# Kernel optimization log

Measured on AMD Instinct MI355X. Metric: run time of the kernel, lower is better.

## Reference

```python
import jax, jax.numpy as jnp
import numpy as np

T, N, E, F_IN, C = 8, 50000, 800000, 64, 64


def setup_inputs() -> dict:
    key = jax.random.key(0)
    ks = jax.random.split(key, 32)
    inp = {
        "x": jax.random.normal(ks[0], (T, N, F_IN), dtype=jnp.float32),
        "edge_index": jax.random.randint(ks[1], (2, E), 0, N, dtype=jnp.int32),
        "edge_weight": jax.random.uniform(ks[2], (E,), dtype=jnp.float32),
    }
    s = 0.05
    names = ["xz", "hz", "xr", "hr", "xh", "hh"]
    for i, nm in enumerate(names):
        cin = F_IN if nm[0] == "x" else C
        inp[f"W{nm}0"] = jax.random.normal(ks[3 + 3 * i], (cin, C), dtype=jnp.float32) * s
        inp[f"W{nm}1"] = jax.random.normal(ks[4 + 3 * i], (cin, C), dtype=jnp.float32) * s
        inp[f"b{nm}"] = jax.random.normal(ks[5 + 3 * i], (C,), dtype=jnp.float32) * s
    inp["W_lin"] = jax.random.normal(ks[30], (C, 1), dtype=jnp.float32) * s
    inp["b_lin"] = jax.random.normal(ks[31], (1,), dtype=jnp.float32) * s
    return inp


def reference(x, edge_index, edge_weight,
              Wxz0, Wxz1, bxz, Whz0, Whz1, bhz,
              Wxr0, Wxr1, bxr, Whr0, Whr1, bhr,
              Wxh0, Wxh1, bxh, Whh0, Whh1, bhh,
              W_lin, b_lin):
    src, dst = edge_index[0], edge_index[1]
    n = x.shape[1]
    # sym-normalized L_hat = -D^{-1/2} A D^{-1/2} (ChebConv, lambda_max=2)
    deg = jnp.zeros((n,), x.dtype).at[src].add(edge_weight)
    dinv = jnp.where(deg > 0, jax.lax.rsqrt(jnp.maximum(deg, 1e-12)), 0.0)
    nw = -edge_weight * dinv[src] * dinv[dst]  # (E,)

    def cheb(v, W0, W1, b):
        # K=2 Chebyshev: v @ W0 + (L_hat v) @ W1 + b ; v: (T, N, Cin)
        msgs = nw[None, :, None] * v[:, src, :]          # (T, E, Cin)
        tx1 = jnp.zeros_like(v).at[:, dst, :].add(msgs)  # scatter-add over nodes
        return v @ W0 + tx1 @ W1 + b

    H = jnp.zeros(x.shape[:2] + (Whz0.shape[0],), x.dtype)  # H=None -> zeros
    Z = jax.nn.sigmoid(cheb(x, Wxz0, Wxz1, bxz) + cheb(H, Whz0, Whz1, bhz))
    R = jax.nn.sigmoid(cheb(x, Wxr0, Wxr1, bxr) + cheb(H, Whr0, Whr1, bhr))
    Ht = jnp.tanh(cheb(x, Wxh0, Wxh1, bxh) + cheb(R * H, Whh0, Whh1, bhh))
    H = Z * H + (1.0 - Z) * Ht
    h = jax.nn.relu(H)
    return h @ W_lin + b_lin
```

## Files before the change

kernel.cpp:

```cpp
#include <hip/hip_runtime.h>

#define T_ 8
#define N_ 50000
#define E_ 800000
#define C_ 64
#define OVF_CAP 131072
#define NB 196
#define NBLK 256
#define EPB 3125
#define SCN (2 * NB * NBLK)
#define SCAN_TILES 49

typedef __attribute__((ext_vector_type(8))) short bf16x8;
typedef __attribute__((ext_vector_type(4))) float f32x4;

__device__ inline short f2bf(float f) {
    union { float f; unsigned int u; } v; v.f = f;
    unsigned int u = v.u + 0x7FFFu + ((v.u >> 16) & 1u);
    return (short)(u >> 16);
}
__device__ inline float bf2f_lo(unsigned int u) {
    union { unsigned int u; float f; } v; v.u = u << 16;
    return v.f;
}
__device__ inline float bf2f_hi(unsigned int u) {
    union { unsigned int u; float f; } v; v.u = u & 0xffff0000u;
    return v.f;
}

__device__ inline void xcvt_step(int id, const float* __restrict__ x,
                                 unsigned short* __restrict__ xb) {
    int c8 = id & 7;
    int t = (id >> 3) & 7;
    int n = id >> 6;
    const float* xr = x + ((long long)t * N_ + n) * C_ + c8 * 8;
    float4 a = *(const float4*)(xr);
    float4 b = *(const float4*)(xr + 4);
    bf16x8 o;
    o[0] = f2bf(a.x); o[1] = f2bf(a.y); o[2] = f2bf(a.z); o[3] = f2bf(a.w);
    o[4] = f2bf(b.x); o[5] = f2bf(b.y); o[6] = f2bf(b.z); o[7] = f2bf(b.w);
    *(bf16x8*)(xb + (long long)id * 8) = o;
}

__global__ __launch_bounds__(256) void prep_kernel(
        const int* __restrict__ src, const int* __restrict__ dst,
        int* __restrict__ counts,
        const float* __restrict__ x, unsigned short* __restrict__ xb,
        const float* __restrict__ Wz0, const float* __restrict__ Wz1,
        const float* __restrict__ Wh0, const float* __restrict__ Wh1,
        short* __restrict__ swz) {
    if (blockIdx.x < NBLK) {
        __shared__ int h[2 * NB];
        int t = threadIdx.x;
        for (int i = t; i < 2 * NB; i += 256) h[i] = 0;
        __syncthreads();
        int e0 = blockIdx.x * EPB;
        for (int j = t; j < EPB; j += 256) {
            int e = e0 + j;
            atomicAdd(&h[src[e] >> 8], 1);
            atomicAdd(&h[NB + (dst[e] >> 8)], 1);
        }
        __syncthreads();
        for (int i = t; i < 2 * NB; i += 256)
            counts[i * NBLK + blockIdx.x] = h[i];
    } else if (blockIdx.x < NBLK + 12500) {
        int id = (blockIdx.x - NBLK) * 256 + threadIdx.x;
        xcvt_step(id, x, xb);
    } else {
        int idx = (blockIdx.x - NBLK - 12500) * 256 + threadIdx.x;
        int j = idx & 7;
        int lane = (idx >> 3) & 63;
        int kb = (idx >> 9) & 1;
        int c = (idx >> 10) & 3;
        int mat = idx >> 12;
        const float* W = (mat == 0) ? Wz0 : (mat == 1) ? Wz1 : (mat == 2) ? Wh0 : Wh1;
        int k = kb * 32 + (lane >> 4) * 8 + j;
        int n = c * 16 + (lane & 15);
        swz[idx] = f2bf(W[k * 64 + n]);
    }
}

__global__ __launch_bounds__(1024) void scan_a_kernel(int* __restrict__ cnts,
                                                      int* __restrict__ tsum) {
    __shared__ int wsum[16];
    int tid = threadIdx.x, lane = tid & 63, wid = tid >> 6;
    int i0 = blockIdx.x * 2048 + tid * 2;
    int v0 = cnts[i0], v1 = cnts[i0 + 1];
    int orig = v0 + v1;
    int v = orig;
#pragma unroll
    for (int off = 1; off < 64; off <<= 1) {
        int u = __shfl_up(v, off);
        if (lane >= off) v += u;
    }
    if (lane == 63) wsum[wid] = v;
    __syncthreads();
    if (wid == 0) {
        int s = (lane < 16) ? wsum[lane] : 0;
#pragma unroll
        for (int off = 1; off < 16; off <<= 1) {
            int u = __shfl_up(s, off);
            if (lane >= off) s += u;
        }
        if (lane < 16) wsum[lane] = s;
    }
    __syncthreads();
    int wpre = wid ? wsum[wid - 1] : 0;
    int ex = wpre + v - orig;
    cnts[i0] = ex;
    cnts[i0 + 1] = ex + v0;
    if (tid == 0) tsum[blockIdx.x] = wsum[15];
}

__global__ __launch_bounds__(1024) void scan_b_kernel(const int* __restrict__ tsum,
                                                      int* __restrict__ cnts) {
    __shared__ int soff[SCAN_TILES];
    int tid = threadIdx.x, lane = tid & 63, wid = tid >> 6;
    if (wid == 0) {
        int own = (lane < SCAN_TILES) ? tsum[lane] : 0;
        int s = own;
#pragma unroll
        for (int off = 1; off < 64; off <<= 1) {
            int u = __shfl_up(s, off);
            if (lane >= off) s += u;
        }
        if (lane < SCAN_TILES) soff[lane] = s - own;
    }
    __syncthreads();
    int off = soff[blockIdx.x];
    int i0 = blockIdx.x * 2048 + tid;
    cnts[i0] += off;
    cnts[i0 + 1024] += off;
}

__global__ __launch_bounds__(256) void scatter_kernel(
        const int* __restrict__ src, const int* __restrict__ dst,
        const float* __restrict__ w, const int* __restrict__ scn,
        int2* __restrict__ rec) {
    __shared__ int offs[2 * NB];
    int t = threadIdx.x;
    for (int i = t; i < 2 * NB; i += 256)
        offs[i] = scn[i * NBLK + blockIdx.x];
    __syncthreads();
    int e0 = blockIdx.x * EPB;
    for (int j = t; j < EPB; j += 256) {
        int e = e0 + j;
        int s = src[e], d = dst[e];
        float wv = w[e];
        int r0 = atomicAdd(&offs[s >> 8], 1);
        rec[r0] = make_int2(s, __float_as_int(wv));
        int r1 = atomicAdd(&offs[NB + (d >> 8)], 1);
        rec[r1] = make_int2(s | ((d & 255) << 16), __float_as_int(wv));
    }
}

__global__ __launch_bounds__(256) void degw_kernel(
        const int2* __restrict__ rec, const int* __restrict__ scn,
        float* __restrict__ degw) {
    __shared__ float acc[256];
    int t = threadIdx.x, b = blockIdx.x;
    acc[t] = 0.f;
    __syncthreads();
    int s0 = scn[b * NBLK];
    int s1 = (b == NB - 1) ? E_ : scn[(b + 1) * NBLK];
    for (int j = s0 + t; j < s1; j += 256) {
        int2 r = rec[j];
        atomicAdd(&acc[r.x & 255], __int_as_float(r.y));
    }
    __syncthreads();
    int node = b * 256 + t;
    if (node < N_) degw[node] = acc[t];
}

__global__ __launch_bounds__(256) void esbuild_kernel(
        const int2* __restrict__ rec, const int* __restrict__ scn,
        const float* __restrict__ degw, int* __restrict__ cnt,
        int2* __restrict__ es, int cap,
        int* __restrict__ ovfcnt, int4* __restrict__ ovf) {
    __shared__ int cl[256];
    __shared__ float di[256];
    int t = threadIdx.x, b = blockIdx.x;
    cl[t] = 0;
    int node = b * 256 + t;
    float dd = (node < N_) ? degw[node] : 0.f;
    di[t] = dd > 0.f ? rsqrtf(fmaxf(dd, 1e-12f)) : 0.f;
    __syncthreads();
    int s0 = scn[(NB + b) * NBLK];
    int s1 = (b == NB - 1) ? 2 * E_ : scn[(NB + b + 1) * NBLK];
    for (int j = s0 + t; j < s1; j += 256) {
        int2 r = rec[j];
        int s = r.x & 0xffff;
        int dl = (r.x >> 16) & 255;
        float ds = degw[s];
        float is = ds > 0.f ? rsqrtf(fmaxf(ds, 1e-12f)) : 0.f;
        float nwv = -__int_as_float(r.y) * is * di[dl];
        int rank = atomicAdd(&cl[dl], 1);
        int d = b * 256 + dl;
        if (rank < cap) {
            es[d * cap + rank] = make_int2(s, __float_as_int(nwv));
        } else {
            int op = atomicAdd(ovfcnt, 1);
            if (op < OVF_CAP) ovf[op] = make_int4(d, s, __float_as_int(nwv), 0);
        }
    }
    __syncthreads();
    if (node < N_) cnt[node] = cl[t];
}

#define ACC8(W, V)                                                       \
    acc[0] += (W) * bf2f_lo((V).x); acc[1] += (W) * bf2f_hi((V).x);      \
    acc[2] += (W) * bf2f_lo((V).y); acc[3] += (W) * bf2f_hi((V).y);      \
    acc[4] += (W) * bf2f_lo((V).z); acc[5] += (W) * bf2f_hi((V).z);      \
    acc[6] += (W) * bf2f_lo((V).w); acc[7] += (W) * bf2f_hi((V).w);

__global__ __launch_bounds__(256) void gather_node_kernel(
        const int* __restrict__ cnt, const int2* __restrict__ es, int cap,
        const int* __restrict__ ovfcnt, const int4* __restrict__ ovf,
        const unsigned short* __restrict__ xb, const short* __restrict__ swz,
        const float* __restrict__ bxz, const float* __restrict__ bhz,
        const float* __restrict__ bxh, const float* __restrict__ bhh,
        const float* __restrict__ Wlin, const float* __restrict__ blin,
        float* __restrict__ out) {
    __shared__ unsigned short ltx[32 * 72];
    __shared__ float laz[2][16][65];

    int lane = threadIdx.x & 63;
    int wid = threadIdx.x >> 6;
    int base = blockIdx.x * 4;

    {
        int d = base + wid;
        int t = lane >> 3;
        int oct = lane & 7;
        int2 pk = (lane < cap) ? es[d * cap + lane] : make_int2(0, 0);
        int m = cnt[d];
        int mb = m < cap ? m : cap;

        float acc[8] = {0.f, 0.f, 0.f, 0.f, 0.f, 0.f, 0.f, 0.f};
        const unsigned short* xbase = xb + lane * 8;
        int k = 0;
        for (; k + 3 < mb; k += 4) {
            int s0 = __shfl(pk.x, k);
            int s1 = __shfl(pk.x, k + 1);
            int s2 = __shfl(pk.x, k + 2);
            int s3 = __shfl(pk.x, k + 3);
            uint4 v0 = *(const uint4*)(xbase + (long long)s0 * 512);
            uint4 v1 = *(const uint4*)(xbase + (long long)s1 * 512);
            uint4 v2 = *(const uint4*)(xbase + (long long)s2 * 512);
            uint4 v3 = *(const uint4*)(xbase + (long long)s3 * 512);
            float w0 = __int_as_float(__shfl(pk.y, k));
            float w1 = __int_as_float(__shfl(pk.y, k + 1));
            float w2 = __int_as_float(__shfl(pk.y, k + 2));
            float w3 = __int_as_float(__shfl(pk.y, k + 3));
            ACC8(w0, v0);
            ACC8(w1, v1);
            ACC8(w2, v2);
            ACC8(w3, v3);
        }
        for (; k < mb; ++k) {
            int s0 = __shfl(pk.x, k);
            float w0 = __int_as_float(__shfl(pk.y, k));
            uint4 v0 = *(const uint4*)(xbase + (long long)s0 * 512);
            ACC8(w0, v0);
        }
        if (m > cap) {
            int oc = *ovfcnt;
            if (oc > OVF_CAP) oc = OVF_CAP;
            for (int i = 0; i < oc; ++i) {
                int4 o = ovf[i];
                if (o.x == d) {
                    float w0 = __int_as_float(o.z);
                    uint4 v0 = *(const uint4*)(xbase + (long long)o.y * 512);
                    ACC8(w0, v0);
                }
            }
        }
        uint4 ob;
        ob.x = (unsigned int)(unsigned short)f2bf(acc[0]) |
               ((unsigned int)(unsigned short)f2bf(acc[1]) << 16);
        ob.y = (unsigned int)(unsigned short)f2bf(acc[2]) |
               ((unsigned int)(unsigned short)f2bf(acc[3]) << 16);
        ob.z = (unsigned int)(unsigned short)f2bf(acc[4]) |
               ((unsigned int)(unsigned short)f2bf(acc[5]) << 16);
        ob.w = (unsigned int)(unsigned short)f2bf(acc[6]) |
               ((unsigned int)(unsigned short)f2bf(acc[7]) << 16);
        int r = wid * 8 + t;
        *(uint4*)(ltx + r * 72 + oct * 8) = ob;
    }
    __syncthreads();

    int mt = wid >> 1;
    int g = wid & 1;
    int c16 = lane & 15;
    int kq = lane >> 4;
    int r_blk = mt * 16 + c16;
    const unsigned short* xr = xb + (long long)(base * 8 + r_blk) * C_ + kq * 8;
    bf16x8 ax0 = *(const bf16x8*)(xr);
    bf16x8 ax1 = *(const bf16x8*)(xr + 32);
    bf16x8 at0 = *(const bf16x8*)(ltx + r_blk * 72 + kq * 8);
    bf16x8 at1 = *(const bf16x8*)(ltx + r_blk * 72 + 32 + kq * 8);

    const float* bA = g ? bxh : bxz;
    const float* bB = g ? bhh : bhz;
    const short* wA = swz + (2 * g) * 4096 + lane * 8;
    const short* wB = swz + (2 * g + 1) * 4096 + lane * 8;

    f32x4 a4[4];
#pragma unroll
    for (int c = 0; c < 4; ++c) {
        int col = c * 16 + c16;
        float bv = bA[col] + bB[col];
        a4[c] = (f32x4){bv, bv, bv, bv};
    }
#pragma unroll
    for (int c = 0; c < 4; ++c) {
        bf16x8 bA0 = *(const bf16x8*)(wA + (c * 2 + 0) * 512);
        bf16x8 bA1 = *(const bf16x8*)(wA + (c * 2 + 1) * 512);
        bf16x8 bB0 = *(const bf16x8*)(wB + (c * 2 + 0) * 512);
        bf16x8 bB1 = *(const bf16x8*)(wB + (c * 2 + 1) * 512);
        a4[c] = __builtin_amdgcn_mfma_f32_16x16x32_bf16(ax0, bA0, a4[c], 0, 0, 0);
        a4[c] = __builtin_amdgcn_mfma_f32_16x16x32_bf16(ax1, bA1, a4[c], 0, 0, 0);
        a4[c] = __builtin_amdgcn_mfma_f32_16x16x32_bf16(at0, bB0, a4[c], 0, 0, 0);
        a4[c] = __builtin_amdgcn_mfma_f32_16x16x32_bf16(at1, bB1, a4[c], 0, 0, 0);
    }

    if (g == 0) {
#pragma unroll
        for (int c = 0; c < 4; ++c)
#pragma unroll
            for (int r = 0; r < 4; ++r)
                laz[mt][kq * 4 + r][c * 16 + c16] = a4[c][r];
    }
    __syncthreads();
    if (g == 1) {
        float part[4] = {0.f, 0.f, 0.f, 0.f};
#pragma unroll
        for (int c = 0; c < 4; ++c) {
            int col = c * 16 + c16;
            float wl = Wlin[col];
#pragma unroll
            for (int r = 0; r < 4; ++r) {
                float a = laz[mt][kq * 4 + r][col];
                float b = a4[c][r];
                float z = 1.f / (1.f + __expf(-a));
                float aa = fabsf(b);
                float e = __expf(-2.f * aa);
                float ht = copysignf((1.f - e) / (1.f + e), b);
                float h = fmaxf((1.f - z) * ht, 0.f);
                part[r] += h * wl;
            }
        }
#pragma unroll
        for (int m = 1; m <= 8; m <<= 1) {
#pragma unroll
            for (int r = 0; r < 4; ++r) part[r] += __shfl_xor(part[r], m);
        }
        if (c16 == 0) {
            float bl = blin[0];
#pragma unroll
            for (int r = 0; r < 4; ++r) {
                int rb = mt * 16 + kq * 4 + r;
                out[(long long)(rb & 7) * N_ + base + (rb >> 3)] = part[r] + bl;
            }
        }
    }
}

extern "C" void kernel_launch(void* const* d_in, const int* in_sizes, int n_in,
                              void* d_out, int out_size, void* d_ws, size_t ws_size,
                              hipStream_t stream) {
    const float* x    = (const float*)d_in[0];
    const int*   ei   = (const int*)d_in[1];
    const float* w    = (const float*)d_in[2];
    const float* Wxz0 = (const float*)d_in[3];
    const float* Wxz1 = (const float*)d_in[4];
    const float* bxz  = (const float*)d_in[5];
    const float* bhz  = (const float*)d_in[8];
    const float* Wxh0 = (const float*)d_in[15];
    const float* Wxh1 = (const float*)d_in[16];
    const float* bxh  = (const float*)d_in[17];
    const float* bhh  = (const float*)d_in[20];
    const float* Wlin = (const float*)d_in[21];
    const float* blin = (const float*)d_in[22];
    float* out = (float*)d_out;

    const int* src = ei;
    const int* dst = ei + E_;

    char* ws = (char*)d_ws;
    size_t off = 0;
    auto alloc = [&](size_t bytes) {
        char* p = ws + off;
        off = (off + bytes + 511) & ~(size_t)511;
        return p;
    };
    short* swz         = (short*)alloc(4 * 4096 * sizeof(short));
    float* degw        = (float*)alloc((size_t)N_ * 4);
    int*   cnt         = (int*)alloc((size_t)N_ * 4);
    int*   ovfcnt      = (int*)alloc(512);
    int4*  ovf         = (int4*)alloc((size_t)OVF_CAP * 16);
    int*   counts      = (int*)alloc((size_t)SCN * 4);
    int*   tsum        = (int*)alloc((size_t)SCAN_TILES * 4);
    int2*  rec         = (int2*)alloc((size_t)2 * E_ * 8);
    unsigned short* xb = (unsigned short*)alloc((size_t)T_ * N_ * C_ * 2);
    size_t fixed = off;

    int cap = 16;
    for (int c : {64, 48, 32, 24}) {
        if (fixed + (size_t)N_ * c * 8 + 512 <= ws_size) { cap = c; break; }
    }
    int2* es = (int2*)alloc((size_t)N_ * cap * 8);

    hipMemsetAsync(ovfcnt, 0, 4, stream);

    prep_kernel<<<NBLK + 12500 + 64, 256, 0, stream>>>(
        src, dst, counts, x, xb, Wxz0, Wxz1, Wxh0, Wxh1, swz);

    scan_a_kernel<<<SCAN_TILES, 1024, 0, stream>>>(counts, tsum);
    scan_b_kernel<<<SCAN_TILES, 1024, 0, stream>>>(tsum, counts);

    scatter_kernel<<<NBLK, 256, 0, stream>>>(src, dst, w, counts, rec);

    degw_kernel<<<NB, 256, 0, stream>>>(rec, counts, degw);

    esbuild_kernel<<<NB, 256, 0, stream>>>(rec, counts, degw, cnt,
                                           es, cap, ovfcnt, ovf);

    gather_node_kernel<<<N_ / 4, 256, 0, stream>>>(
        cnt, es, cap, ovfcnt, ovf, xb, swz,
        bxz, bhz, bxh, bhh, Wlin, blin, out);
}
```

Before: 368.1 us.

## Stage scatter records in LDS, widen preprocessing blocks, fold memset, split gather launch

The scatter kernel now builds a per-block local histogram and prefix sum, writes records into shared memory first, then copies them to global memory in bucket-contiguous runs. This turns random global writes into mostly coalesced ones. degw, esbuild and scatter move to 1024-thread blocks, the overflow counter reset is folded into scan_b in place of a separate memset, and the gather kernel is split into two half-size launches. The LDS staging buffer (about 50KB) limits occupancy, and the extra launch adds overhead.

```diff
diff --git a/kernel.cpp b/kernel.cpp
--- a/kernel.cpp
+++ b/kernel.cpp
@@ -113,9 +113,11 @@
 }
 
 __global__ __launch_bounds__(1024) void scan_b_kernel(const int* __restrict__ tsum,
-                                                      int* __restrict__ cnts) {
+                                                      int* __restrict__ cnts,
+                                                      int* __restrict__ ovfcnt) {
     __shared__ int soff[SCAN_TILES];
     int tid = threadIdx.x, lane = tid & 63, wid = tid >> 6;
+    if (blockIdx.x == 0 && tid == 0) *ovfcnt = 0;
     if (wid == 0) {
         int own = (lane < SCAN_TILES) ? tsum[lane] : 0;
         int s = own;
@@ -133,46 +135,83 @@
     cnts[i0 + 1024] += off;
 }
 
-__global__ __launch_bounds__(256) void scatter_kernel(
+__global__ __launch_bounds__(1024) void scatter_kernel(
         const int* __restrict__ src, const int* __restrict__ dst,
         const float* __restrict__ w, const int* __restrict__ scn,
         int2* __restrict__ rec) {
-    __shared__ int offs[2 * NB];
-    int t = threadIdx.x;
-    for (int i = t; i < 2 * NB; i += 256)
-        offs[i] = scn[i * NBLK + blockIdx.x];
-    __syncthreads();
-    int e0 = blockIdx.x * EPB;
-    for (int j = t; j < EPB; j += 256) {
+    __shared__ int h[512];
+    __shared__ int delta[512];
+    __shared__ int wsum[8];
+    __shared__ int2 lrec[2 * EPB];
+    int t = threadIdx.x, lane = t & 63, wid = t >> 6;
+    int c = blockIdx.x;
+    if (t < 512) h[t] = 0;
+    __syncthreads();
+    int e0 = c * EPB;
+    for (int j = t; j < EPB; j += 1024) {
+        int e = e0 + j;
+        atomicAdd(&h[src[e] >> 8], 1);
+        atomicAdd(&h[NB + (dst[e] >> 8)], 1);
+    }
+    __syncthreads();
+    int v = (t < 512) ? h[t] : 0;
+    int s2 = v;
+#pragma unroll
+    for (int off = 1; off < 64; off <<= 1) {
+        int u = __shfl_up(s2, off);
+        if (lane >= off) s2 += u;
+    }
+    if (lane == 63 && wid < 8) wsum[wid] = s2;
+    __syncthreads();
+    if (t == 0) {
+        int r = 0;
+#pragma unroll
+        for (int i = 0; i < 8; ++i) { int x2 = wsum[i]; wsum[i] = r; r += x2; }
+    }
+    __syncthreads();
+    int ex = (t < 512) ? (wsum[wid] + s2 - v) : 0;
+    int gb = (t < 2 * NB) ? scn[t * NBLK + c] : 0;
+    __syncthreads();
+    if (t < 512) { delta[t] = gb - ex; h[t] = ex; }
+    __syncthreads();
+    int lb196 = h[NB];
+    __syncthreads();
+    for (int j = t; j < EPB; j += 1024) {
         int e = e0 + j;
         int s = src[e], d = dst[e];
-        float wv = w[e];
-        int r0 = atomicAdd(&offs[s >> 8], 1);
-        rec[r0] = make_int2(s, __float_as_int(wv));
-        int r1 = atomicAdd(&offs[NB + (d >> 8)], 1);
-        rec[r1] = make_int2(s | ((d & 255) << 16), __float_as_int(wv));
-    }
-}
-
-__global__ __launch_bounds__(256) void degw_kernel(
+        int wv = __float_as_int(w[e]);
+        int p0 = atomicAdd(&h[s >> 8], 1);
+        lrec[p0] = make_int2(s, wv);
+        int p1 = atomicAdd(&h[NB + (d >> 8)], 1);
+        lrec[p1] = make_int2(s | ((d & 255) << 16) | ((d >> 8) << 24), wv);
+    }
+    __syncthreads();
+    for (int j = t; j < 2 * EPB; j += 1024) {
+        int2 r = lrec[j];
+        int i = (j >= lb196) ? (NB + ((unsigned)r.x >> 24)) : ((r.x & 0xffff) >> 8);
+        rec[delta[i] + j] = r;
+    }
+}
+
+__global__ __launch_bounds__(1024) void degw_kernel(
         const int2* __restrict__ rec, const int* __restrict__ scn,
         float* __restrict__ degw) {
     __shared__ float acc[256];
     int t = threadIdx.x, b = blockIdx.x;
-    acc[t] = 0.f;
+    if (t < 256) acc[t] = 0.f;
     __syncthreads();
     int s0 = scn[b * NBLK];
-    int s1 = (b == NB - 1) ? E_ : scn[(b + 1) * NBLK];
-    for (int j = s0 + t; j < s1; j += 256) {
+    int s1 = scn[(b + 1) * NBLK];
+    for (int j = s0 + t; j < s1; j += 1024) {
         int2 r = rec[j];
         atomicAdd(&acc[r.x & 255], __int_as_float(r.y));
     }
     __syncthreads();
     int node = b * 256 + t;
-    if (node < N_) degw[node] = acc[t];
-}
-
-__global__ __launch_bounds__(256) void esbuild_kernel(
+    if (t < 256 && node < N_) degw[node] = acc[t];
+}
+
+__global__ __launch_bounds__(1024) void esbuild_kernel(
         const int2* __restrict__ rec, const int* __restrict__ scn,
         const float* __restrict__ degw, int* __restrict__ cnt,
         int2* __restrict__ es, int cap,
@@ -180,14 +219,16 @@
     __shared__ int cl[256];
     __shared__ float di[256];
     int t = threadIdx.x, b = blockIdx.x;
-    cl[t] = 0;
     int node = b * 256 + t;
-    float dd = (node < N_) ? degw[node] : 0.f;
-    di[t] = dd > 0.f ? rsqrtf(fmaxf(dd, 1e-12f)) : 0.f;
+    if (t < 256) {
+        cl[t] = 0;
+        float dd = (node < N_) ? degw[node] : 0.f;
+        di[t] = dd > 0.f ? rsqrtf(fmaxf(dd, 1e-12f)) : 0.f;
+    }
     __syncthreads();
     int s0 = scn[(NB + b) * NBLK];
     int s1 = (b == NB - 1) ? 2 * E_ : scn[(NB + b + 1) * NBLK];
-    for (int j = s0 + t; j < s1; j += 256) {
+    for (int j = s0 + t; j < s1; j += 1024) {
         int2 r = rec[j];
         int s = r.x & 0xffff;
         int dl = (r.x >> 16) & 255;
@@ -204,7 +245,7 @@
         }
     }
     __syncthreads();
-    if (node < N_) cnt[node] = cl[t];
+    if (t < 256 && node < N_) cnt[node] = cl[t];
 }
 
 #define ACC8(W, V)                                                       \
@@ -220,13 +261,13 @@
         const float* __restrict__ bxz, const float* __restrict__ bhz,
         const float* __restrict__ bxh, const float* __restrict__ bhh,
         const float* __restrict__ Wlin, const float* __restrict__ blin,
-        float* __restrict__ out) {
+        float* __restrict__ out, int boff) {
     __shared__ unsigned short ltx[32 * 72];
     __shared__ float laz[2][16][65];
 
     int lane = threadIdx.x & 63;
     int wid = threadIdx.x >> 6;
-    int base = blockIdx.x * 4;
+    int base = (blockIdx.x + boff) * 4;
 
     {
         int d = base + wid;
@@ -411,22 +452,23 @@
     }
     int2* es = (int2*)alloc((size_t)N_ * cap * 8);
 
-    hipMemsetAsync(ovfcnt, 0, 4, stream);
-
     prep_kernel<<<NBLK + 12500 + 64, 256, 0, stream>>>(
         src, dst, counts, x, xb, Wxz0, Wxz1, Wxh0, Wxh1, swz);
 
     scan_a_kernel<<<SCAN_TILES, 1024, 0, stream>>>(counts, tsum);
-    scan_b_kernel<<<SCAN_TILES, 1024, 0, stream>>>(tsum, counts);
-
-    scatter_kernel<<<NBLK, 256, 0, stream>>>(src, dst, w, counts, rec);
-
-    degw_kernel<<<NB, 256, 0, stream>>>(rec, counts, degw);
-
-    esbuild_kernel<<<NB, 256, 0, stream>>>(rec, counts, degw, cnt,
-                                           es, cap, ovfcnt, ovf);
-
-    gather_node_kernel<<<N_ / 4, 256, 0, stream>>>(
+    scan_b_kernel<<<SCAN_TILES, 1024, 0, stream>>>(tsum, counts, ovfcnt);
+
+    scatter_kernel<<<NBLK, 1024, 0, stream>>>(src, dst, w, counts, rec);
+
+    degw_kernel<<<NB, 1024, 0, stream>>>(rec, counts, degw);
+
+    esbuild_kernel<<<NB, 1024, 0, stream>>>(rec, counts, degw, cnt,
+                                            es, cap, ovfcnt, ovf);
+
+    gather_node_kernel<<<6250, 256, 0, stream>>>(
         cnt, es, cap, ovfcnt, ovf, xb, swz,
-        bxz, bhz, bxh, bhh, Wlin, blin, out);
-}
+        bxz, bhz, bxh, bhh, Wlin, blin, out, 0);
+    gather_node_kernel<<<6250, 256, 0, stream>>>(
+        cnt, es, cap, ovfcnt, ovf, xb, swz,
+        bxz, bhz, bxh, bhh, Wlin, blin, out, 6250);
+}
```

Result: no change. 367.9 us (-0.0%).
